# Kernel tuning notes

Hardware: AMD Instinct MI355X
Metric: run time of the kernel (lower is better)

Reference implementation:

```python
import jax, jax.numpy as jnp
import numpy as np

EPS = 1e-4
HEADS = 8
DIM_HEAD = 32
BALANCE = 0.3


def _normalize(x, dims):
    # torch normalize(): norm over `dims` in fp32; norm = eps + norm*sqrt(norm.numel()/x.numel())
    red = 1
    for d in dims:
        red *= x.shape[d]
    norm = jnp.sqrt(jnp.sum(jnp.square(x.astype(jnp.float32)), axis=dims, keepdims=True))
    norm = EPS + norm / np.sqrt(red)
    return x / norm.astype(x.dtype)


def _mpconv1x1(x, w, gain=1.0):
    # MPConv forward (eval mode): weight-normalize per output channel, scale, 1x1 conv
    w = w.astype(jnp.float32)
    w = _normalize(w, (1, 2, 3))
    fan_in = w.shape[1] * w.shape[2] * w.shape[3]
    w = (w * (gain / np.sqrt(fan_in))).astype(x.dtype)[:, :, 0, 0]  # [out, in]
    return jnp.einsum('oi,nihw->nohw', w, x)


def setup_inputs() -> dict:
    key = jax.random.key(0)
    k1, k2, k3 = jax.random.split(key, 3)
    x = jax.random.normal(k1, (2, 256, 48, 48), dtype=jnp.float32)
    w_qkv = jax.random.normal(k2, (768, 256, 1, 1), dtype=jnp.float32)
    w_out = jax.random.normal(k3, (256, 256, 1, 1), dtype=jnp.float32)
    return {"x": x, "w_qkv": w_qkv, "w_out": w_out}


def reference(x, w_qkv, w_out):
    n, c, h, w_sp = x.shape
    seq = h * w_sp
    y = _mpconv1x1(x, w_qkv)                          # [n, 3c, h, w]
    y = y.reshape(n, HEADS, DIM_HEAD, 3, seq)         # channel split: head x dim_head x 3
    y = _normalize(y, (2,))                           # L2-normalize over dim_head axis
    q = y[:, :, :, 0, :]
    k = y[:, :, :, 1, :]
    v = y[:, :, :, 2, :]
    # scores [n, h, q, k] with k scaled by 1/sqrt(dim_head)
    att = jax.nn.softmax(jnp.einsum('nhcq,nhck->nhqk', q, k) / np.sqrt(DIM_HEAD), axis=3)
    y = jnp.einsum('nhqk,nhck->nhcq', att, v)         # [n, heads, dim_head, seq]
    y = _mpconv1x1(y.reshape(n, c, h, w_sp), w_out)
    t = BALANCE
    # mp_sum: lerp then magnitude-preserving rescale
    return (x + t * (y - x)) / np.sqrt((1 - t) ** 2 + t ** 2)
```

## Files before the change

### kernel.cpp

```cpp
#include <hip/hip_runtime.h>
#include <math.h>

#define EPSN 1e-4f
#define SEQ 2304

using bf16x8 = __attribute__((ext_vector_type(8))) short;
using f32x4  = __attribute__((ext_vector_type(4))) float;

__device__ inline unsigned short f2bf(float x) {
    union { float f; unsigned u; } c; c.f = x;
    unsigned u = c.u;
    u += 0x7fffu + ((u >> 16) & 1u);
    return (unsigned short)(u >> 16);
}

__device__ inline unsigned cvt_pk_bf16(float lo, float hi) {
    unsigned r;
    asm("v_cvt_pk_bf16_f32 %0, %1, %2" : "=v"(r) : "v"(lo), "v"(hi));
    return r;
}

__global__ __launch_bounds__(256) void prep_kernel(const float* __restrict__ w_qkv,
                                                   const float* __restrict__ w_out,
                                                   const float* __restrict__ x,
                                                   unsigned short* __restrict__ wqb,
                                                   unsigned short* __restrict__ wob,
                                                   unsigned short* __restrict__ xt) {
    __shared__ __align__(16) unsigned short T[64][80];
    __shared__ float red[4];
    __shared__ float scale_s;
    int bid = blockIdx.x;
    if (bid < 1024) {
        const float* src;
        unsigned short* dst;
        if (bid < 768) { src = w_qkv + bid * 256; dst = wqb + bid * 256; }
        else           { src = w_out + (bid - 768) * 256; dst = wob + (bid - 768) * 256; }
        float v = src[threadIdx.x];
        float ss = v * v;
        for (int off = 32; off > 0; off >>= 1) ss += __shfl_down(ss, off, 64);
        int lane = threadIdx.x & 63, wid = threadIdx.x >> 6;
        if (lane == 0) red[wid] = ss;
        __syncthreads();
        if (threadIdx.x == 0) {
            float t = red[0] + red[1] + red[2] + red[3];
            scale_s = 1.0f / (sqrtf(t) + 16.0f * EPSN);
        }
        __syncthreads();
        dst[threadIdx.x] = f2bf(v * scale_s);
    } else {
        int e0 = bid - 1024;
        int st = e0 % 36, ct = (e0 / 36) & 3, n = e0 / 144;
        int t = threadIdx.x;
#pragma unroll
        for (int p = 0; p < 4; ++p) {
            int e = t + p * 256;
            int c = e >> 4, sv = (e & 15) * 4;
            float4 v = *(const float4*)&x[(size_t)(n * 256 + ct * 64 + c) * SEQ + st * 64 + sv];
            T[sv + 0][c] = f2bf(v.x);
            T[sv + 1][c] = f2bf(v.y);
            T[sv + 2][c] = f2bf(v.z);
            T[sv + 3][c] = f2bf(v.w);
        }
        __syncthreads();
#pragma unroll
        for (int p = 0; p < 2; ++p) {
            int e = t + p * 256;
            int s = e >> 3, cb = (e & 7) * 8;
            uint4 v = *(const uint4*)&T[s][cb];
            *(uint4*)&xt[(size_t)(n * SEQ + st * 64 + s) * 256 + ct * 64 + cb] = v;
        }
    }
}

__global__ __launch_bounds__(256) void qkv_fused_kernel(const unsigned short* __restrict__ xt,
                                                        const unsigned short* __restrict__ wqb,
                                                        unsigned short* __restrict__ qn,
                                                        unsigned short* __restrict__ kn,
                                                        unsigned short* __restrict__ vn) {
    __shared__ float Cs[96][65];
    int h  = blockIdx.x;
    int st = blockIdx.y;
    int n  = blockIdx.z;
    int tid = threadIdx.x;
    int wave = tid >> 6, lane = tid & 63;
    int ln = lane & 15, quad = lane >> 4;
    const unsigned short* Abase = wqb + (size_t)(h * 96 + ln) * 256 + quad * 8;
    const unsigned short* Bbase = xt + (size_t)(n * SEQ + st * 64 + wave * 16 + ln) * 256 + quad * 8;
    f32x4 acc[6];
#pragma unroll
    for (int m = 0; m < 6; ++m) acc[m] = (f32x4){0.f, 0.f, 0.f, 0.f};
#pragma unroll
    for (int kc = 0; kc < 8; ++kc) {
        bf16x8 b = *(const bf16x8*)(Bbase + kc * 32);
#pragma unroll
        for (int m = 0; m < 6; ++m) {
            bf16x8 a = *(const bf16x8*)(Abase + (size_t)(m * 16) * 256 + kc * 32);
            acc[m] = __builtin_amdgcn_mfma_f32_16x16x32_bf16(a, b, acc[m], 0, 0, 0);
        }
    }
#pragma unroll
    for (int m = 0; m < 6; ++m)
#pragma unroll
        for (int r = 0; r < 4; ++r)
            Cs[m * 16 + quad * 4 + r][wave * 16 + ln] = acc[m][r];
    __syncthreads();
    if (tid < 192) {
        int sl = tid & 63, wh = tid >> 6;
        int s = st * 64 + sl;
        int nh = n * 8 + h;
        float v[32];
        float ss = 0.f;
#pragma unroll
        for (int d = 0; d < 32; ++d) { v[d] = Cs[3 * d + wh][sl]; ss += v[d] * v[d]; }
        float inv = 1.0f / (EPSN + sqrtf(ss * (1.0f / 32.0f)));
        if (wh == 0) inv *= 0.17677669529663687f * 1.4426950408889634f;
        if (wh == 2) {
            unsigned short* dst = vn + (size_t)nh * 73728 + s;
#pragma unroll
            for (int d = 0; d < 32; ++d) dst[(size_t)d * SEQ] = f2bf(v[d] * inv);
        } else {
            unsigned short* dst = (wh == 1 ? kn : qn) + (size_t)nh * 73728 + (size_t)s * 32;
            unsigned wbuf[16];
#pragma unroll
            for (int j = 0; j < 16; ++j)
                wbuf[j] = (unsigned)f2bf(v[2 * j] * inv) | ((unsigned)f2bf(v[2 * j + 1] * inv) << 16);
#pragma unroll
            for (int j = 0; j < 4; ++j) {
                uint4 t4 = make_uint4(wbuf[4 * j], wbuf[4 * j + 1], wbuf[4 * j + 2], wbuf[4 * j + 3]);
                *(uint4*)(dst + j * 8) = t4;
            }
        }
    }
}

__global__ __launch_bounds__(256) void attn_mfma_kernel(const unsigned short* __restrict__ qn,
                                                        const unsigned short* __restrict__ kn,
                                                        const unsigned short* __restrict__ vn,
                                                        float* __restrict__ Opart,
                                                        float* __restrict__ Lpart) {
    __shared__ __align__(16) unsigned short Ks[2][64][40];
    __shared__ __align__(16) unsigned short Vs[2][32][72];
    __shared__ __align__(16) unsigned short Ps[4][16][72];
    int tid = threadIdx.x;
    int wave = tid >> 6, lane = tid & 63;
    int ln = lane & 15, quad = lane >> 4;
    int qt = blockIdx.x, nh = blockIdx.y, kz = blockIdx.z;
    const unsigned short* Qg = qn + (size_t)nh * 73728;
    const unsigned short* Kg = kn + (size_t)nh * 73728;
    const unsigned short* Vg = vn + (size_t)nh * 73728;

    bf16x8 qf = *(const bf16x8*)(Qg + (size_t)(qt * 64 + wave * 16 + ln) * 32 + quad * 8);
    bf16x8 ones;
#pragma unroll
    for (int i = 0; i < 8; ++i) ones[i] = (short)0x3F80;

    f32x4 o0 = {0.f, 0.f, 0.f, 0.f};
    f32x4 o1 = {0.f, 0.f, 0.f, 0.f};
    f32x4 lac = {0.f, 0.f, 0.f, 0.f};

    int kt0 = kz * 12;
    uint4 kreg = *(const uint4*)(Kg + (size_t)(kt0 * 64) * 32 + tid * 8);
    uint4 vreg = *(const uint4*)(Vg + (size_t)(tid >> 3) * SEQ + kt0 * 64 + (tid & 7) * 8);
    *(uint4*)(&Ks[0][tid >> 2][(tid & 3) * 8]) = kreg;
    *(uint4*)(&Vs[0][tid >> 3][(tid & 7) * 8]) = vreg;

    for (int i = 0; i < 12; ++i) {
        int buf = i & 1;
        if (i + 1 < 12) {
            int k0n = (kt0 + i + 1) * 64;
            kreg = *(const uint4*)(Kg + (size_t)k0n * 32 + tid * 8);
            vreg = *(const uint4*)(Vg + (size_t)(tid >> 3) * SEQ + k0n + (tid & 7) * 8);
        }
        __syncthreads();

        const f32x4 zero = {0.f, 0.f, 0.f, 0.f};
#pragma unroll
        for (int c = 0; c < 4; ++c) {
            bf16x8 kf = *(const bf16x8*)(&Ks[buf][c * 16 + ln][quad * 8]);
            f32x4 sc = __builtin_amdgcn_mfma_f32_16x16x32_bf16(kf, qf, zero, 0, 0, 0);
            unsigned w0 = cvt_pk_bf16(exp2f(sc[0]), exp2f(sc[1]));
            unsigned w1 = cvt_pk_bf16(exp2f(sc[2]), exp2f(sc[3]));
            *(uint2*)(&Ps[wave][ln][c * 16 + quad * 4]) = make_uint2(w0, w1);
        }
#pragma unroll
        for (int kc = 0; kc < 2; ++kc) {
            bf16x8 pf = *(const bf16x8*)(&Ps[wave][ln][kc * 32 + quad * 8]);
            bf16x8 v0 = *(const bf16x8*)(&Vs[buf][ln][kc * 32 + quad * 8]);
            bf16x8 v1 = *(const bf16x8*)(&Vs[buf][16 + ln][kc * 32 + quad * 8]);
            lac = __builtin_amdgcn_mfma_f32_16x16x32_bf16(pf, ones, lac, 0, 0, 0);
            o0  = __builtin_amdgcn_mfma_f32_16x16x32_bf16(pf, v0, o0, 0, 0, 0);
            o1  = __builtin_amdgcn_mfma_f32_16x16x32_bf16(pf, v1, o1, 0, 0, 0);
        }
        if (i + 1 < 12) {
            *(uint4*)(&Ks[buf ^ 1][tid >> 2][(tid & 3) * 8]) = kreg;
            *(uint4*)(&Vs[buf ^ 1][tid >> 3][(tid & 7) * 8]) = vreg;
        }
    }

    float* Ob = Opart + ((size_t)(kz * 16 + nh) * 36 + qt) * 2048;
    float* Lb = Lpart + ((size_t)(kz * 16 + nh) * 36 + qt) * 64;
#pragma unroll
    for (int r = 0; r < 4; ++r) {
        int ql = wave * 16 + quad * 4 + r;
        Ob[ql * 32 + ln]      = o0[r];
        Ob[ql * 32 + 16 + ln] = o1[r];
        if (ln == 0) Lb[ql] = lac[r];
    }
}

__global__ __launch_bounds__(256) void attn_reduce_kernel(const float* __restrict__ Opart,
                                                          const float* __restrict__ Lpart,
                                                          unsigned short* __restrict__ y2t) {
    int qt = blockIdx.x, nh = blockIdx.y;
    int n = nh >> 3, h = nh & 7;
    size_t s0 = (size_t)nh * 36 + qt;
    const float* O0 = Opart + s0 * 2048;
    const float* O1 = Opart + (s0 + 36 * 16) * 2048;
    const float* O2 = Opart + (s0 + 72 * 16) * 2048;
    const float* L0 = Lpart + s0 * 64;
    const float* L1 = Lpart + (s0 + 36 * 16) * 64;
    const float* L2 = Lpart + (s0 + 72 * 16) * 64;
#pragma unroll
    for (int p = 0; p < 2; ++p) {
        int idx = (threadIdx.x + p * 256) * 4;
        int q = idx >> 5, c = idx & 31;
        float inv = 1.0f / (L0[q] + L1[q] + L2[q]);
        float4 a = *(const float4*)&O0[idx];
        float4 b = *(const float4*)&O1[idx];
        float4 d = *(const float4*)&O2[idx];
        unsigned w0 = (unsigned)f2bf((a.x + b.x + d.x) * inv) |
                      ((unsigned)f2bf((a.y + b.y + d.y) * inv) << 16);
        unsigned w1 = (unsigned)f2bf((a.z + b.z + d.z) * inv) |
                      ((unsigned)f2bf((a.w + b.w + d.w) * inv) << 16);
        *(uint2*)&y2t[((size_t)(n * SEQ) + qt * 64 + q) * 256 + h * 32 + c] = make_uint2(w0, w1);
    }
}

__global__ __launch_bounds__(256) void out_gemm_kernel(const unsigned short* __restrict__ y2t,
                                                       const unsigned short* __restrict__ wob,
                                                       const float* __restrict__ x,
                                                       float* __restrict__ out) {
    int mt = blockIdx.x;
    int st = blockIdx.y;
    int n  = blockIdx.z;
    int tid = threadIdx.x;
    int wave = tid >> 6, lane = tid & 63;
    int ln = lane & 15, quad = lane >> 4;
    int m0 = mt * 64 + wave * 16;
    const unsigned short* Abase = wob + (size_t)(m0 + ln) * 256 + quad * 8;
    const unsigned short* Bbase = y2t + (size_t)(n * SEQ + st * 32 + ln) * 256 + quad * 8;
    f32x4 acc[2];
#pragma unroll
    for (int c = 0; c < 2; ++c) acc[c] = (f32x4){0.f, 0.f, 0.f, 0.f};
#pragma unroll
    for (int kc = 0; kc < 8; ++kc) {
        bf16x8 a = *(const bf16x8*)(Abase + kc * 32);
#pragma unroll
        for (int c = 0; c < 2; ++c) {
            bf16x8 b = *(const bf16x8*)(Bbase + (size_t)(c * 16) * 256 + kc * 32);
            acc[c] = __builtin_amdgcn_mfma_f32_16x16x32_bf16(a, b, acc[c], 0, 0, 0);
        }
    }
    const float c0f = 0.7f * 1.3130643285972254f;
    const float c1f = 0.3f * 1.3130643285972254f;
#pragma unroll
    for (int c = 0; c < 2; ++c)
#pragma unroll
        for (int r = 0; r < 4; ++r) {
            int o = m0 + quad * 4 + r;
            int s = st * 32 + c * 16 + ln;
            size_t idx = (size_t)(n * 256 + o) * SEQ + s;
            out[idx] = c0f * x[idx] + c1f * acc[c][r];
        }
}

extern "C" void kernel_launch(void* const* d_in, const int* in_sizes, int n_in,
                              void* d_out, int out_size, void* d_ws, size_t ws_size,
                              hipStream_t stream) {
    (void)in_sizes; (void)n_in; (void)out_size; (void)ws_size;
    const float* x     = (const float*)d_in[0];
    const float* w_qkv = (const float*)d_in[1];
    const float* w_out = (const float*)d_in[2];
    float* out = (float*)d_out;
    float* ws  = (float*)d_ws;
    unsigned short* wqb = (unsigned short*)(ws);
    unsigned short* wob = (unsigned short*)(ws + 98304);
    unsigned short* xt  = (unsigned short*)(ws + 131072);
    unsigned short* y2t = (unsigned short*)(ws + 131072);
    unsigned short* qn  = (unsigned short*)(ws + 720896);
    unsigned short* kn  = (unsigned short*)(ws + 1310720);
    unsigned short* vn  = (unsigned short*)(ws + 1900544);
    float* Opart = ws + 2490368;
    float* Lpart = ws + 6029312;

    hipLaunchKernelGGL(prep_kernel, dim3(1312), dim3(256), 0, stream,
                       w_qkv, w_out, x, wqb, wob, xt);
    hipLaunchKernelGGL(qkv_fused_kernel, dim3(8, 36, 2), dim3(256), 0, stream,
                       xt, wqb, qn, kn, vn);
    hipLaunchKernelGGL(attn_mfma_kernel, dim3(36, 16, 3), dim3(256), 0, stream,
                       qn, kn, vn, Opart, Lpart);
    hipLaunchKernelGGL(attn_reduce_kernel, dim3(36, 16), dim3(256), 0, stream,
                       Opart, Lpart, y2t);
    hipLaunchKernelGGL(out_gemm_kernel, dim3(4, 72, 2), dim3(256), 0, stream,
                       y2t, wob, x, out);
}
```

Measured before the change: 133.2 us.

## Drop split-K attention and fuse normalization into attention kernel; vectorize weight prep

The attention kernel no longer splits the key dimension three ways. Each block now loops over all 36 key tiles, normalizes by the row sum in-kernel and writes bf16 output through shared memory. This removes the separate reduce kernel and the fp32 partial buffers, at the cost of a grid 3x smaller (576 blocks) with longer serial loops. Weight normalization in prep now handles one row per wave with float4 loads and xor-shuffle reduction, needing fewer blocks and no block syncs.

```diff
diff --git a/kernel.cpp b/kernel.cpp
--- a/kernel.cpp
+++ b/kernel.cpp
@@ -27,28 +27,23 @@
                                                    unsigned short* __restrict__ wob,
                                                    unsigned short* __restrict__ xt) {
     __shared__ __align__(16) unsigned short T[64][80];
-    __shared__ float red[4];
-    __shared__ float scale_s;
     int bid = blockIdx.x;
-    if (bid < 1024) {
+    if (bid < 256) {
+        int wave = threadIdx.x >> 6, lane = threadIdx.x & 63;
+        int row = bid * 4 + wave;
         const float* src;
         unsigned short* dst;
-        if (bid < 768) { src = w_qkv + bid * 256; dst = wqb + bid * 256; }
-        else           { src = w_out + (bid - 768) * 256; dst = wob + (bid - 768) * 256; }
-        float v = src[threadIdx.x];
-        float ss = v * v;
-        for (int off = 32; off > 0; off >>= 1) ss += __shfl_down(ss, off, 64);
-        int lane = threadIdx.x & 63, wid = threadIdx.x >> 6;
-        if (lane == 0) red[wid] = ss;
-        __syncthreads();
-        if (threadIdx.x == 0) {
-            float t = red[0] + red[1] + red[2] + red[3];
-            scale_s = 1.0f / (sqrtf(t) + 16.0f * EPSN);
-        }
-        __syncthreads();
-        dst[threadIdx.x] = f2bf(v * scale_s);
+        if (row < 768) { src = w_qkv + (size_t)row * 256; dst = wqb + (size_t)row * 256; }
+        else           { src = w_out + (size_t)(row - 768) * 256; dst = wob + (size_t)(row - 768) * 256; }
+        float4 v = *(const float4*)&src[lane * 4];
+        float ss = v.x * v.x + v.y * v.y + v.z * v.z + v.w * v.w;
+        for (int off = 32; off > 0; off >>= 1) ss += __shfl_xor(ss, off, 64);
+        float sc = 1.0f / (sqrtf(ss) + 16.0f * EPSN);
+        unsigned p0 = (unsigned)f2bf(v.x * sc) | ((unsigned)f2bf(v.y * sc) << 16);
+        unsigned p1 = (unsigned)f2bf(v.z * sc) | ((unsigned)f2bf(v.w * sc) << 16);
+        *(uint2*)&dst[lane * 4] = make_uint2(p0, p1);
     } else {
-        int e0 = bid - 1024;
+        int e0 = bid - 256;
         int st = e0 % 36, ct = (e0 / 36) & 3, n = e0 / 144;
         int t = threadIdx.x;
 #pragma unroll
@@ -136,15 +131,16 @@
 __global__ __launch_bounds__(256) void attn_mfma_kernel(const unsigned short* __restrict__ qn,
                                                         const unsigned short* __restrict__ kn,
                                                         const unsigned short* __restrict__ vn,
-                                                        float* __restrict__ Opart,
-                                                        float* __restrict__ Lpart) {
+                                                        unsigned short* __restrict__ y2t) {
     __shared__ __align__(16) unsigned short Ks[2][64][40];
     __shared__ __align__(16) unsigned short Vs[2][32][72];
     __shared__ __align__(16) unsigned short Ps[4][16][72];
+    __shared__ float Os[64][33];
     int tid = threadIdx.x;
     int wave = tid >> 6, lane = tid & 63;
     int ln = lane & 15, quad = lane >> 4;
-    int qt = blockIdx.x, nh = blockIdx.y, kz = blockIdx.z;
+    int qt = blockIdx.x, nh = blockIdx.y;
+    int n = nh >> 3, h = nh & 7;
     const unsigned short* Qg = qn + (size_t)nh * 73728;
     const unsigned short* Kg = kn + (size_t)nh * 73728;
     const unsigned short* Vg = vn + (size_t)nh * 73728;
@@ -158,16 +154,15 @@
     f32x4 o1 = {0.f, 0.f, 0.f, 0.f};
     f32x4 lac = {0.f, 0.f, 0.f, 0.f};
 
-    int kt0 = kz * 12;
-    uint4 kreg = *(const uint4*)(Kg + (size_t)(kt0 * 64) * 32 + tid * 8);
-    uint4 vreg = *(const uint4*)(Vg + (size_t)(tid >> 3) * SEQ + kt0 * 64 + (tid & 7) * 8);
+    uint4 kreg = *(const uint4*)(Kg + (size_t)0 + tid * 8);
+    uint4 vreg = *(const uint4*)(Vg + (size_t)(tid >> 3) * SEQ + (tid & 7) * 8);
     *(uint4*)(&Ks[0][tid >> 2][(tid & 3) * 8]) = kreg;
     *(uint4*)(&Vs[0][tid >> 3][(tid & 7) * 8]) = vreg;
 
-    for (int i = 0; i < 12; ++i) {
+    for (int i = 0; i < 36; ++i) {
         int buf = i & 1;
-        if (i + 1 < 12) {
-            int k0n = (kt0 + i + 1) * 64;
+        if (i + 1 < 36) {
+            int k0n = (i + 1) * 64;
             kreg = *(const uint4*)(Kg + (size_t)k0n * 32 + tid * 8);
             vreg = *(const uint4*)(Vg + (size_t)(tid >> 3) * SEQ + k0n + (tid & 7) * 8);
         }
@@ -191,48 +186,29 @@
             o0  = __builtin_amdgcn_mfma_f32_16x16x32_bf16(pf, v0, o0, 0, 0, 0);
             o1  = __builtin_amdgcn_mfma_f32_16x16x32_bf16(pf, v1, o1, 0, 0, 0);
         }
-        if (i + 1 < 12) {
+        if (i + 1 < 36) {
             *(uint4*)(&Ks[buf ^ 1][tid >> 2][(tid & 3) * 8]) = kreg;
             *(uint4*)(&Vs[buf ^ 1][tid >> 3][(tid & 7) * 8]) = vreg;
         }
     }
 
-    float* Ob = Opart + ((size_t)(kz * 16 + nh) * 36 + qt) * 2048;
-    float* Lb = Lpart + ((size_t)(kz * 16 + nh) * 36 + qt) * 64;
 #pragma unroll
     for (int r = 0; r < 4; ++r) {
-        int ql = wave * 16 + quad * 4 + r;
-        Ob[ql * 32 + ln]      = o0[r];
-        Ob[ql * 32 + 16 + ln] = o1[r];
-        if (ln == 0) Lb[ql] = lac[r];
-    }
-}
-
-__global__ __launch_bounds__(256) void attn_reduce_kernel(const float* __restrict__ Opart,
-                                                          const float* __restrict__ Lpart,
-                                                          unsigned short* __restrict__ y2t) {
-    int qt = blockIdx.x, nh = blockIdx.y;
-    int n = nh >> 3, h = nh & 7;
-    size_t s0 = (size_t)nh * 36 + qt;
-    const float* O0 = Opart + s0 * 2048;
-    const float* O1 = Opart + (s0 + 36 * 16) * 2048;
-    const float* O2 = Opart + (s0 + 72 * 16) * 2048;
-    const float* L0 = Lpart + s0 * 64;
-    const float* L1 = Lpart + (s0 + 36 * 16) * 64;
-    const float* L2 = Lpart + (s0 + 72 * 16) * 64;
-#pragma unroll
-    for (int p = 0; p < 2; ++p) {
-        int idx = (threadIdx.x + p * 256) * 4;
-        int q = idx >> 5, c = idx & 31;
-        float inv = 1.0f / (L0[q] + L1[q] + L2[q]);
-        float4 a = *(const float4*)&O0[idx];
-        float4 b = *(const float4*)&O1[idx];
-        float4 d = *(const float4*)&O2[idx];
-        unsigned w0 = (unsigned)f2bf((a.x + b.x + d.x) * inv) |
-                      ((unsigned)f2bf((a.y + b.y + d.y) * inv) << 16);
-        unsigned w1 = (unsigned)f2bf((a.z + b.z + d.z) * inv) |
-                      ((unsigned)f2bf((a.w + b.w + d.w) * inv) << 16);
-        *(uint2*)&y2t[((size_t)(n * SEQ) + qt * 64 + q) * 256 + h * 32 + c] = make_uint2(w0, w1);
+        int q = wave * 16 + quad * 4 + r;
+        float inv = 1.0f / lac[r];
+        Os[q][ln]      = o0[r] * inv;
+        Os[q][16 + ln] = o1[r] * inv;
+    }
+    __syncthreads();
+    {
+        int q = tid >> 2, dg = tid & 3;
+        const float* row = &Os[q][dg * 8];
+        unsigned u0 = (unsigned)f2bf(row[0]) | ((unsigned)f2bf(row[1]) << 16);
+        unsigned u1 = (unsigned)f2bf(row[2]) | ((unsigned)f2bf(row[3]) << 16);
+        unsigned u2 = (unsigned)f2bf(row[4]) | ((unsigned)f2bf(row[5]) << 16);
+        unsigned u3 = (unsigned)f2bf(row[6]) | ((unsigned)f2bf(row[7]) << 16);
+        *(uint4*)&y2t[((size_t)(n * SEQ) + qt * 64 + q) * 256 + h * 32 + dg * 8] =
+            make_uint4(u0, u1, u2, u3);
     }
 }
 
@@ -290,17 +266,13 @@
     unsigned short* qn  = (unsigned short*)(ws + 720896);
     unsigned short* kn  = (unsigned short*)(ws + 1310720);
     unsigned short* vn  = (unsigned short*)(ws + 1900544);
-    float* Opart = ws + 2490368;
-    float* Lpart = ws + 6029312;
-
-    hipLaunchKernelGGL(prep_kernel, dim3(1312), dim3(256), 0, stream,
+
+    hipLaunchKernelGGL(prep_kernel, dim3(544), dim3(256), 0, stream,
                        w_qkv, w_out, x, wqb, wob, xt);
     hipLaunchKernelGGL(qkv_fused_kernel, dim3(8, 36, 2), dim3(256), 0, stream,
                        xt, wqb, qn, kn, vn);
-    hipLaunchKernelGGL(attn_mfma_kernel, dim3(36, 16, 3), dim3(256), 0, stream,
-                       qn, kn, vn, Opart, Lpart);
-    hipLaunchKernelGGL(attn_reduce_kernel, dim3(36, 16), dim3(256), 0, stream,
-                       Opart, Lpart, y2t);
+    hipLaunchKernelGGL(attn_mfma_kernel, dim3(36, 16), dim3(256), 0, stream,
+                       qn, kn, vn, y2t);
     hipLaunchKernelGGL(out_gemm_kernel, dim3(4, 72, 2), dim3(256), 0, stream,
                        y2t, wob, x, out);
 }
```

Measured after the change: 138.0 us. 3.6% more time.
